# Kernel optimization log

Hardware: AMD Instinct MI355X
Metric: run time of the kernel (lower is better)

## Reference

```python
import jax, jax.numpy as jnp
import numpy as np

DIM = 64
SQRT_DIM = np.sqrt(DIM).astype(np.float32)
NEG_INF = -1e9


def setup_inputs() -> dict:
    key = jax.random.key(0)
    kq, kk, kv, km = jax.random.split(key, 4)
    B, Q, K, D = 32, 1024, 1024, DIM
    query = jax.random.normal(kq, (B, Q, D), dtype=jnp.float32)
    k = jax.random.normal(kk, (B, K, D), dtype=jnp.float32)
    value = jax.random.normal(kv, (B, K, D), dtype=jnp.float32)
    mask = jax.random.randint(km, (B, Q, K), 0, 2).astype(jnp.bool_)
    return {"query": query, "key": k, "value": value, "mask": mask}


def reference(query, key, value, mask):
    # score: [B, Q, K]
    score = jnp.einsum('bqd,bkd->bqk', query, key) / SQRT_DIM
    score = jnp.where(mask, NEG_INF, score)
    attn = jax.nn.softmax(score, axis=-1)
    context = jnp.einsum('bqk,bkd->bqd', attn, value)
    return (context, attn)
```

## Files before the change

kernel.cpp:

```cpp
#include <hip/hip_runtime.h>

constexpr int BATCH = 32;
constexpr int QLEN  = 1024;
constexpr int KLEN  = 1024;
constexpr int DIM   = 64;
constexpr int TQ    = 16;

typedef float    f32x4 __attribute__((ext_vector_type(4)));
typedef int      i32x4 __attribute__((ext_vector_type(4)));
typedef _Float16 f16x8 __attribute__((ext_vector_type(8)));
typedef _Float16 f16x4 __attribute__((ext_vector_type(4)));

__device__ __forceinline__ f16x8 cvt_h8(f32x4 a, f32x4 b) {
  f16x8 h;
  h[0] = (_Float16)a[0]; h[1] = (_Float16)a[1]; h[2] = (_Float16)a[2]; h[3] = (_Float16)a[3];
  h[4] = (_Float16)b[0]; h[5] = (_Float16)b[1]; h[6] = (_Float16)b[2]; h[7] = (_Float16)b[3];
  return h;
}

__device__ __forceinline__ int swz(int r, int c) {
  return (r << 10) + (c ^ ((r & 7) << 3));
}

constexpr int TK = 128;
__global__ __launch_bounds__(256)
void vt_kernel(const float* __restrict__ V, _Float16* __restrict__ Vt) {
  __shared__ _Float16 lt[DIM][TK + 8];
  const int b = blockIdx.y, k0 = blockIdx.x * TK;
  const int t = threadIdx.x;
  const int d4 = (t & 15) * 4;
  #pragma unroll
  for (int p = 0; p < TK / 16; ++p) {
    const int kl = (t >> 4) + p * 16;
    const f32x4 v = *(const f32x4*)(V + ((size_t)(b * KLEN + k0 + kl)) * DIM + d4);
    #pragma unroll
    for (int j = 0; j < 4; ++j) lt[d4 + j][kl] = (_Float16)v[j];
  }
  __syncthreads();
  const int d = t >> 2;
  #pragma unroll
  for (int j2 = 0; j2 < TK / 32; ++j2) {
    const int seg = (t & 3) + j2 * 4;
    *(f16x8*)(Vt + (size_t)b * DIM * KLEN + (size_t)d * KLEN + k0 + seg * 8) =
        *(const f16x8*)(&lt[d][seg * 8]);
  }
}

__global__ __launch_bounds__(256, 5)
void sdpa_kernel(const float* __restrict__ Qg, const float* __restrict__ Kg,
                 const _Float16* __restrict__ Vt, const int* __restrict__ Mg,
                 float* __restrict__ Ctx, float* __restrict__ Attn)
{
  __shared__ __attribute__((aligned(16))) _Float16 sc[TQ * 1024];

  const int tid  = threadIdx.x;
  const int w    = tid >> 6;
  const int l    = tid & 63;
  const int n16  = l & 15;
  const int quad = l >> 4;

  const int lin  = blockIdx.y * gridDim.x + blockIdx.x;
  const int nlin = (lin & 7) * (BATCH * (QLEN / TQ) / 8) + (lin >> 3);
  const int b    = nlin >> 6;
  const int q0   = (nlin & 63) * TQ;

  const int* mrow0 = Mg + ((size_t)(b * QLEN + q0 + w * 4)) * KLEN;
  i32x4 mva[4][4];
  #pragma unroll
  for (int j = 0; j < 4; ++j)
    #pragma unroll
    for (int c = 0; c < 4; ++c)
      mva[j][c] = __builtin_nontemporal_load((const i32x4*)(mrow0 + j * KLEN + c * 256 + l * 4));

  const float* qbase = Qg + ((size_t)(b * QLEN + q0 + n16)) * DIM + quad * 8;
  const f16x8 aq0 = cvt_h8(*(const f32x4*)(qbase),      *(const f32x4*)(qbase + 4));
  const f16x8 aq1 = cvt_h8(*(const f32x4*)(qbase + 32), *(const f32x4*)(qbase + 36));

  #pragma unroll 4
  for (int kc = 0; kc < 16; ++kc) {
    const int col = w * 256 + kc * 16 + n16;
    const float* kbase = Kg + ((size_t)(b * KLEN + col)) * DIM + quad * 8;
    const f16x8 bk0 = cvt_h8(*(const f32x4*)(kbase),      *(const f32x4*)(kbase + 4));
    const f16x8 bk1 = cvt_h8(*(const f32x4*)(kbase + 32), *(const f32x4*)(kbase + 36));
    f32x4 acc = {0.f, 0.f, 0.f, 0.f};
    acc = __builtin_amdgcn_mfma_f32_16x16x32_f16(aq0, bk0, acc, 0, 0, 0);
    acc = __builtin_amdgcn_mfma_f32_16x16x32_f16(aq1, bk1, acc, 0, 0, 0);
    #pragma unroll
    for (int i = 0; i < 4; ++i)
      sc[swz(quad * 4 + i, col)] = (_Float16)acc[i];
  }
  __syncthreads();

  #pragma unroll
  for (int j = 0; j < 4; ++j) {
    const int r = w * 4 + j;
    float s[16];
    float sum = 0.f;
    #pragma unroll
    for (int c = 0; c < 4; ++c) {
      const f16x4 hv = *(const f16x4*)(&sc[swz(r, c * 256 + l * 4)]);
      #pragma unroll
      for (int u = 0; u < 4; ++u) {
        const float e = __expf((float)hv[u] * 0.125f);
        s[c * 4 + u] = mva[j][c][u] ? 0.f : e;
        sum += s[c * 4 + u];
      }
    }
    #pragma unroll
    for (int d = 1; d < 64; d <<= 1) sum += __shfl_xor(sum, d, 64);
    const float inv = __builtin_amdgcn_rcpf(sum);
    float* arow = Attn + ((size_t)(b * QLEN + q0 + r)) * KLEN;
    #pragma unroll
    for (int c = 0; c < 4; ++c) {
      f32x4 pv = { s[c*4+0] * inv, s[c*4+1] * inv, s[c*4+2] * inv, s[c*4+3] * inv };
      __builtin_nontemporal_store(pv, (f32x4*)(arow + c * 256 + l * 4));
      f16x4 hp = { (_Float16)pv[0], (_Float16)pv[1], (_Float16)pv[2], (_Float16)pv[3] };
      *(f16x4*)(&sc[swz(r, c * 256 + l * 4)]) = hp;
    }
  }
  __syncthreads();

  const _Float16* vtb = Vt + (size_t)b * DIM * KLEN + (size_t)(w * 16 + n16) * KLEN;
  f32x4 cacc = {0.f, 0.f, 0.f, 0.f};
  #pragma unroll 4
  for (int kk = 0; kk < 32; ++kk) {
    const f16x8 ap = *(const f16x8*)(&sc[swz(n16, kk * 32 + quad * 8)]);
    const f16x8 bv = *(const f16x8*)(vtb + kk * 32 + quad * 8);
    cacc = __builtin_amdgcn_mfma_f32_16x16x32_f16(ap, bv, cacc, 0, 0, 0);
  }
  float* cbase = Ctx + ((size_t)(b * QLEN + q0 + quad * 4)) * DIM + w * 16 + n16;
  #pragma unroll
  for (int i = 0; i < 4; ++i) cbase[(size_t)i * DIM] = cacc[i];
}

extern "C" void kernel_launch(void* const* d_in, const int* in_sizes, int n_in,
                              void* d_out, int out_size, void* d_ws, size_t ws_size,
                              hipStream_t stream) {
  const float* Qg = (const float*)d_in[0];
  const float* Kg = (const float*)d_in[1];
  const float* Vg = (const float*)d_in[2];
  const int*   Mg = (const int*)d_in[3];
  float* Ctx  = (float*)d_out;
  float* Attn = (float*)d_out + (size_t)BATCH * QLEN * DIM;
  _Float16* Vt = (_Float16*)d_ws;

  dim3 tgrid(KLEN / TK, BATCH);
  vt_kernel<<<tgrid, 256, 0, stream>>>(Vg, Vt);

  dim3 grid(QLEN / TQ, BATCH);
  sdpa_kernel<<<grid, 256, 0, stream>>>(Qg, Kg, Vt, Mg, Ctx, Attn);
}
```

Before: 330.5 us.

## Pack boolean mask into bitmask in a pre-pass kernel

Adds a kernel that reads the int32 mask and packs each row into 16 64-bit ballot words in workspace. The attention kernel then reads these bit words instead of holding the full mask in registers, which cuts register pressure. It also changes the attention stores from nontemporal to normal and lowers the occupancy hint. The mask is still fully read, now in a separate serialized pass, which adds a launch and breaks overlap with the compute.

```diff
diff --git a/kernel.cpp b/kernel.cpp
--- a/kernel.cpp
+++ b/kernel.cpp
@@ -46,9 +46,30 @@
   }
 }
 
-__global__ __launch_bounds__(256, 5)
+__global__ __launch_bounds__(256)
+void maskpack_kernel(const int* __restrict__ Mg, unsigned long long* __restrict__ Mp) {
+  const int l  = threadIdx.x & 63;
+  const int gw = blockIdx.x * 4 + (threadIdx.x >> 6);
+  for (int row = gw; row < BATCH * QLEN; row += 8192) {
+    const int* mr = Mg + (size_t)row * KLEN;
+    unsigned long long myw = 0;
+    #pragma unroll
+    for (int c = 0; c < 4; ++c) {
+      const i32x4 v = __builtin_nontemporal_load((const i32x4*)(mr + c * 256 + l * 4));
+      #pragma unroll
+      for (int u = 0; u < 4; ++u) {
+        const unsigned long long bl = __ballot(v[u] != 0);
+        if (l == c * 4 + u) myw = bl;
+      }
+    }
+    if (l < 16) Mp[(size_t)row * 16 + l] = myw;
+  }
+}
+
+__global__ __launch_bounds__(256, 4)
 void sdpa_kernel(const float* __restrict__ Qg, const float* __restrict__ Kg,
-                 const _Float16* __restrict__ Vt, const int* __restrict__ Mg,
+                 const _Float16* __restrict__ Vt,
+                 const unsigned long long* __restrict__ Mp,
                  float* __restrict__ Ctx, float* __restrict__ Attn)
 {
   __shared__ __attribute__((aligned(16))) _Float16 sc[TQ * 1024];
@@ -63,14 +84,6 @@
   const int nlin = (lin & 7) * (BATCH * (QLEN / TQ) / 8) + (lin >> 3);
   const int b    = nlin >> 6;
   const int q0   = (nlin & 63) * TQ;
-
-  const int* mrow0 = Mg + ((size_t)(b * QLEN + q0 + w * 4)) * KLEN;
-  i32x4 mva[4][4];
-  #pragma unroll
-  for (int j = 0; j < 4; ++j)
-    #pragma unroll
-    for (int c = 0; c < 4; ++c)
-      mva[j][c] = __builtin_nontemporal_load((const i32x4*)(mrow0 + j * KLEN + c * 256 + l * 4));
 
   const float* qbase = Qg + ((size_t)(b * QLEN + q0 + n16)) * DIM + quad * 8;
   const f16x8 aq0 = cvt_h8(*(const f32x4*)(qbase),      *(const f32x4*)(qbase + 4));
@@ -94,6 +107,7 @@
   #pragma unroll
   for (int j = 0; j < 4; ++j) {
     const int r = w * 4 + j;
+    const unsigned long long* mpr = Mp + (size_t)(b * QLEN + q0 + r) * 16;
     float s[16];
     float sum = 0.f;
     #pragma unroll
@@ -102,7 +116,7 @@
       #pragma unroll
       for (int u = 0; u < 4; ++u) {
         const float e = __expf((float)hv[u] * 0.125f);
-        s[c * 4 + u] = mva[j][c][u] ? 0.f : e;
+        s[c * 4 + u] = ((mpr[c * 4 + u] >> l) & 1ULL) ? 0.f : e;
         sum += s[c * 4 + u];
       }
     }
@@ -113,7 +127,7 @@
     #pragma unroll
     for (int c = 0; c < 4; ++c) {
       f32x4 pv = { s[c*4+0] * inv, s[c*4+1] * inv, s[c*4+2] * inv, s[c*4+3] * inv };
-      __builtin_nontemporal_store(pv, (f32x4*)(arow + c * 256 + l * 4));
+      *(f32x4*)(arow + c * 256 + l * 4) = pv;
       f16x4 hp = { (_Float16)pv[0], (_Float16)pv[1], (_Float16)pv[2], (_Float16)pv[3] };
       *(f16x4*)(&sc[swz(r, c * 256 + l * 4)]) = hp;
     }
@@ -143,10 +157,14 @@
   float* Ctx  = (float*)d_out;
   float* Attn = (float*)d_out + (size_t)BATCH * QLEN * DIM;
   _Float16* Vt = (_Float16*)d_ws;
+  unsigned long long* Mp =
+      (unsigned long long*)((char*)d_ws + (size_t)BATCH * DIM * KLEN * 2);
 
   dim3 tgrid(KLEN / TK, BATCH);
   vt_kernel<<<tgrid, 256, 0, stream>>>(Vg, Vt);
 
+  maskpack_kernel<<<2048, 256, 0, stream>>>(Mg, Mp);
+
   dim3 grid(QLEN / TQ, BATCH);
-  sdpa_kernel<<<grid, 256, 0, stream>>>(Qg, Kg, Vt, Mg, Ctx, Attn);
+  sdpa_kernel<<<grid, 256, 0, stream>>>(Qg, Kg, Vt, Mp, Ctx, Attn);
 }
```

Result: no change. 329.3 us (-0.4%).
